# Kernel tuning notes

Hardware: AMD Instinct MI355X
Metric: run time of the kernel (lower is better)

Reference implementation:

```python
import jax, jax.numpy as jnp
import numpy as np

DIM = 256; HEADS = 8; HD = DIM // HEADS; WIN = 3; LOCAL = WIN * WIN
SR = 8; SHARED = 4; ROUTED = 2
B = 4; RES = 64; TBL = 4096
EPS = 1.1920929e-07  # torch.finfo(float32).eps


def _l2(x):
    return x / jnp.clip(jnp.linalg.norm(x, axis=-1, keepdims=True), EPS)


def _forward(x, relative_coords_table, q_w, q_b, kv_w, kv_b, temperature,
             query_embedding, rpb_local, learnable_tokens, learnable_bias,
             cpb1_w, cpb1_b, cpb2_w, cpb2_b, sr_w, sr_b, norm_g, norm_b,
             wg_w, wg0_w, wg1_w, proj_w, proj_b, relative_pos_index, H, W):
    B_, N, C = x.shape
    pH, pW = H // SR, W // SR
    PL = pH * pW
    _x = x.reshape(B_ * N, C)

    # ---- MoE head routing: top-k gating over routed heads ----
    gates = jax.nn.softmax(_x @ wg_w.T, axis=1)                 # (BN, n_routed)
    _, idx = jax.lax.top_k(gates, ROUTED)
    mask = jax.nn.one_hot(idx, gates.shape[1], dtype=gates.dtype).sum(axis=1)
    rg = gates * mask
    rg = rg / jnp.clip(jnp.sum(rg, axis=1, keepdims=True), EPS)
    routed_gates = rg.reshape(B_, N, -1) * ROUTED

    # ---- seq-length-scale buffer: log(local valid-window count + pool_len) ----
    r = WIN // 2
    ch = np.minimum(np.arange(H) + r, H - 1) - np.maximum(np.arange(H) - r, 0) + 1
    cw = np.minimum(np.arange(W) + r, W - 1) - np.maximum(np.arange(W) - r, 0) + 1
    sls = jnp.asarray(np.log(np.outer(ch, cw).reshape(-1, 1).astype(np.float32) + PL))

    # ---- queries ----
    q = (x @ q_w.T + q_b).reshape(B_, N, HEADS, HD).transpose(0, 2, 1, 3)
    q_norm = _l2(q)                                             # (B,h,N,d)
    q_scaled = (q_norm + query_embedding) * jax.nn.softplus(temperature) * sls

    # ---- local branch: unfold normalized k and v over 3x3 windows (zero pad) ----
    kv = x @ kv_w.T + kv_b                                      # (B,N,2C)
    k_loc = _l2(kv[..., :C].reshape(B_, N, HEADS, HD)).reshape(B_, N, C)
    kvl = jnp.concatenate([k_loc, kv[..., C:]], -1).transpose(0, 2, 1).reshape(B_, 2 * C, H, W)
    kvp = jnp.pad(kvl, ((0, 0), (0, 0), (r, r), (r, r)))
    patches = jnp.stack([kvp[:, :, i:i + H, j:j + W] for i in range(WIN) for j in range(WIN)], axis=2)
    patches = patches.reshape(B_, 2 * HEADS, HD, LOCAL, N).transpose(0, 1, 4, 2, 3)  # (B,2h,N,d,L)
    k_local, v_local = patches[:, :HEADS], patches[:, HEADS:]

    attn_local = jnp.einsum('bhnd,bhndl->bhnl', q_scaled, k_local) + rpb_local[:, None, :]

    # ---- pooled global branch ----
    x_ = x.transpose(0, 2, 1).reshape(B_, C, H, W)
    x_ = jnp.einsum('oc,bchw->bohw', sr_w, x_) + sr_b[None, :, None, None]  # 1x1 conv
    x_ = jax.nn.gelu(x_, approximate=False)
    x_ = x_.reshape(B_, C, pH, SR, pW, SR).mean((3, 5)).reshape(B_, C, PL).transpose(0, 2, 1)
    mu = x_.mean(-1, keepdims=True)
    var = ((x_ - mu) ** 2).mean(-1, keepdims=True)
    x_ = (x_ - mu) / jnp.sqrt(var + 1e-5) * norm_g + norm_b
    kvp2 = (x_ @ kv_w.T + kv_b).reshape(B_, PL, 2 * HEADS, HD).transpose(0, 2, 1, 3)
    k_pool, v_pool = kvp2[:, :HEADS], kvp2[:, HEADS:]

    cpb = jax.nn.relu(relative_coords_table @ cpb1_w.T + cpb1_b) @ cpb2_w.T + cpb2_b  # (T,h)
    pool_bias = cpb.T[:, relative_pos_index.reshape(-1)].reshape(HEADS, N, PL)
    attn_pool = jnp.einsum('bhnd,bhpd->bhnp', q_scaled, _l2(k_pool)) + pool_bias

    # ---- joint softmax over local + pooled keys ----
    attn = jax.nn.softmax(jnp.concatenate([attn_local, attn_pool], axis=-1), axis=-1)
    a_loc, a_pool = attn[..., :LOCAL], attn[..., LOCAL:]
    a_loc = jnp.einsum('bhnd,hdl->bhnl', q_norm, learnable_tokens) + learnable_bias + a_loc
    x_local = jnp.einsum('bhnl,bhndl->bhnd', a_loc, v_local)
    x_pool = jnp.einsum('bhnp,bhpd->bhnd', a_pool, v_pool)
    out = (x_local + x_pool).transpose(0, 2, 1, 3)              # (B,N,h,d)

    # ---- combine shared + routed head gates ----
    shared_gates = jax.nn.softmax(_x @ wg1_w.T, axis=1).reshape(B_, N, SHARED) * SHARED
    w0 = jax.nn.softmax(_x @ wg0_w.T, axis=1).reshape(B_, N, 2) * 2
    masked = jnp.concatenate([w0[..., 0:1] * shared_gates, w0[..., 1:2] * routed_gates], axis=-1)
    out = (masked[..., None] * out).reshape(B_, N, C)
    return out @ proj_w.T + proj_b


def setup_inputs() -> dict:
    key = jax.random.key(0)
    ks = jax.random.split(key, 20)
    H = W = RES
    N = H * W
    C = DIM
    PL = (H // SR) * (W // SR)

    def nrm(i, shape, s=0.02):
        return jax.random.normal(ks[i], shape, dtype=jnp.float32) * s

    return {
        'x': jax.random.normal(ks[0], (B, N, C), dtype=jnp.float32),
        'relative_coords_table': jax.random.normal(ks[1], (TBL, 2), dtype=jnp.float32),
        'q_w': nrm(3, (C, C)), 'q_b': jnp.zeros((C,), jnp.float32),
        'kv_w': nrm(4, (2 * C, C)), 'kv_b': jnp.zeros((2 * C,), jnp.float32),
        'temperature': jnp.full((HEADS, 1, 1), float(np.log(np.exp(1 / 0.24) - 1)), jnp.float32),
        'query_embedding': nrm(5, (HEADS, 1, HD)),
        'rpb_local': nrm(6, (HEADS, LOCAL), 0.0004),
        'learnable_tokens': nrm(7, (HEADS, HD, LOCAL)),
        'learnable_bias': jnp.zeros((HEADS, 1, LOCAL), jnp.float32),
        'cpb1_w': nrm(8, (512, 2)), 'cpb1_b': jnp.zeros((512,), jnp.float32),
        'cpb2_w': nrm(9, (HEADS, 512)), 'cpb2_b': jnp.zeros((HEADS,), jnp.float32),
        'sr_w': nrm(10, (C, C)), 'sr_b': jnp.zeros((C,), jnp.float32),
        'norm_g': jnp.ones((C,), jnp.float32), 'norm_b': jnp.zeros((C,), jnp.float32),
        'wg_w': nrm(11, (HEADS - SHARED, C)),
        'wg0_w': nrm(12, (2, C)),
        'wg1_w': nrm(13, (SHARED, C)),
        'proj_w': nrm(14, (C, C)), 'proj_b': jnp.zeros((C,), jnp.float32),
        'relative_pos_index': jax.random.randint(ks[2], (N, PL), 0, TBL, dtype=jnp.int32),
        'H': H, 'W': W,
    }


def reference(x, relative_coords_table, q_w, q_b, kv_w, kv_b, temperature,
              query_embedding, rpb_local, learnable_tokens, learnable_bias,
              cpb1_w, cpb1_b, cpb2_w, cpb2_b, sr_w, sr_b, norm_g, norm_b,
              wg_w, wg0_w, wg1_w, proj_w, proj_b, relative_pos_index, H, W):
    return _forward(x, relative_coords_table, q_w, q_b, kv_w, kv_b, temperature,
                    query_embedding, rpb_local, learnable_tokens, learnable_bias,
                    cpb1_w, cpb1_b, cpb2_w, cpb2_b, sr_w, sr_b, norm_g, norm_b,
                    wg_w, wg0_w, wg1_w, proj_w, proj_b, relative_pos_index, H, W)
```

## Files before the change

### kernel.cpp

```cpp
#include <hip/hip_runtime.h>
#include <math.h>

#define EPSF 1.1920929e-07f

typedef __attribute__((ext_vector_type(8))) short short8;
typedef __attribute__((ext_vector_type(4))) float f32x4;

static __device__ __forceinline__ unsigned short f2bf(float f) {
    unsigned int u = __float_as_uint(f);
    return (unsigned short)((u + 0x7FFFu + ((u >> 16) & 1u)) >> 16);
}
static __device__ __forceinline__ float bf2f(unsigned short u) {
    return __uint_as_float((unsigned int)u << 16);
}

__global__ __launch_bounds__(256) void prep_kernel(
    const float* __restrict__ x,
    const float* __restrict__ wg,  const float* __restrict__ wg0,
    const float* __restrict__ wg1,
    const float* __restrict__ q_w, const float* __restrict__ kv_w,
    const float* __restrict__ sr_w, const float* __restrict__ pw,
    const float* __restrict__ tbl,
    const float* __restrict__ c1w, const float* __restrict__ c1b,
    const float* __restrict__ c2w, const float* __restrict__ c2b,
    unsigned short* __restrict__ xbf, float* __restrict__ gate,
    unsigned short* __restrict__ wcat, unsigned short* __restrict__ pwbf,
    float* __restrict__ kv_wT, float* __restrict__ cpb)
{
    __shared__ float shpad[512];
    const int blk = blockIdx.x;
    const int t   = threadIdx.x;
    if (blk < 4096) {
        const int j = t & 63;
        const int row = (blk << 2) + (t >> 6);
        float4 v = *(const float4*)(x + (size_t)row*256 + j*4);
        ushort4 o;
        o.x = f2bf(v.x); o.y = f2bf(v.y); o.z = f2bf(v.z); o.w = f2bf(v.w);
        *(ushort4*)(xbf + (size_t)row*256 + j*4) = o;
        float d[10];
#pragma unroll
        for (int f = 0; f < 10; ++f) {
            const float* wf = (f < 4) ? (wg + f*256) : (f < 6) ? (wg0 + (f-4)*256)
                                                               : (wg1 + (f-6)*256);
            float4 wv = *(const float4*)(wf + j*4);
            float s = v.x*wv.x + v.y*wv.y + v.z*wv.z + v.w*wv.w;
            s += __shfl_xor(s, 32); s += __shfl_xor(s, 16); s += __shfl_xor(s, 8);
            s += __shfl_xor(s, 4);  s += __shfl_xor(s, 2);  s += __shfl_xor(s, 1);
            d[f] = s;
        }
        if (j == 0) {
            float e[4];
            float m = fmaxf(fmaxf(d[0],d[1]), fmaxf(d[2],d[3]));
            float ssum = 0.f;
            for (int i = 0; i < 4; ++i) { e[i] = expf(d[i]-m); ssum += e[i]; }
            for (int i = 0; i < 4; ++i) e[i] /= ssum;
            int i1 = 0;
            for (int i = 1; i < 4; ++i) if (e[i] > e[i1]) i1 = i;
            int i2 = -1;
            for (int i = 0; i < 4; ++i) if (i != i1 && (i2 < 0 || e[i] > e[i2])) i2 = i;
            float rs = fmaxf(e[i1] + e[i2], EPSF);
            float rg[4] = {0.f,0.f,0.f,0.f};
            rg[i1] = e[i1] / rs * 2.f;
            rg[i2] = e[i2] / rs * 2.f;
            float sh[4];
            float m1 = fmaxf(fmaxf(d[6],d[7]), fmaxf(d[8],d[9]));
            float s1 = 0.f;
            for (int i = 0; i < 4; ++i) { sh[i] = expf(d[6+i]-m1); s1 += sh[i]; }
            float mm = fmaxf(d[4], d[5]);
            float e0 = expf(d[4]-mm), e1 = expf(d[5]-mm);
            float w00 = e0/(e0+e1)*2.f, w01 = e1/(e0+e1)*2.f;
            float* gr = gate + ((size_t)row << 3);
            for (int i = 0; i < 4; ++i) gr[i]   = w00 * (sh[i]/s1*4.f);
            for (int i = 0; i < 4; ++i) gr[4+i] = w01 * rg[i];
        }
    } else if (blk < 4416) {
        const int e = ((blk - 4096)*256 + t)*4;
        if (e < 262144) {
            int n = e >> 8, k = e & 255;
            const float* src = (n < 256) ? (q_w + n*256) :
                               (n < 768) ? (kv_w + (n-256)*256) : (sr_w + (n-768)*256);
            float4 v = *(const float4*)(src + k);
            ushort4 o;
            o.x = f2bf(v.x); o.y = f2bf(v.y); o.z = f2bf(v.z); o.w = f2bf(v.w);
            *(ushort4*)(wcat + e) = o;
        } else {
            int e2 = e - 262144;
            float4 v = *(const float4*)(pw + e2);
            ushort4 o;
            o.x = f2bf(v.x); o.y = f2bf(v.y); o.z = f2bf(v.z); o.w = f2bf(v.w);
            *(ushort4*)(pwbf + e2) = o;
        }
    } else if (blk < 4544) {
        const int e = ((blk - 4416)*256 + t)*4;
        int o = e >> 8, k = e & 255;
        float4 v = *(const float4*)(kv_w + e);
        kv_wT[(k+0)*512 + o] = v.x;
        kv_wT[(k+1)*512 + o] = v.y;
        kv_wT[(k+2)*512 + o] = v.z;
        kv_wT[(k+3)*512 + o] = v.w;
    } else {
        const int r = blk - 4544;
        const float c0 = tbl[(size_t)r*2], c1 = tbl[(size_t)r*2+1];
        for (int i = t; i < 512; i += 256)
            shpad[i] = fmaxf(c0*c1w[i*2] + c1*c1w[i*2+1] + c1b[i], 0.f);
        __syncthreads();
        const int hh = t >> 5, dd = t & 31;
        float s = 0.f;
        for (int i = dd; i < 512; i += 32) s += shpad[i] * c2w[hh*512+i];
        for (int off = 16; off; off >>= 1) s += __shfl_xor(s, off, 32);
        if (dd == 0) cpb[(size_t)hh*4096 + r] = (s + c2b[hh]) * 1.44269504089f;
    }
}

__global__ __launch_bounds__(256) void gemm_mfma(
    const unsigned short* __restrict__ A,
    const unsigned short* __restrict__ W,
    const float* __restrict__ B0, const float* __restrict__ B1,
    const float* __restrict__ B2,
    int r1, int r2, int mode,
    float* __restrict__ C, int ldc,
    unsigned short* __restrict__ qkv,
    const float* __restrict__ temp, const float* __restrict__ qe)
{
    __shared__ __attribute__((aligned(16))) unsigned short Bt[64*264];
    const int m0b = blockIdx.y << 7;
    const int n0  = blockIdx.x << 6;
    const int t   = threadIdx.x;
    const int w   = t >> 6;
    const int col16 = t & 15;
    const int quad  = (t & 63) >> 4;

    const float* Bp; int noff;
    if (n0 < r1)      { Bp = B0; noff = 0;  }
    else if (n0 < r2) { Bp = B1; noff = r1; }
    else              { Bp = B2; noff = r2; }

    short8 afrA[8];
    {
        const unsigned short* ap = A + (size_t)(m0b + w*16 + col16)*256 + quad*8;
#pragma unroll
        for (int kk = 0; kk < 8; ++kk)
            afrA[kk] = *(const short8*)(ap + kk*32);
    }
#pragma unroll
    for (int j = 0; j < 8; ++j) {
        int ci = j*256 + t;
        int r = ci >> 5, c = ci & 31;
        uint4 bv = *(const uint4*)(W + (size_t)(n0 + r)*256 + c*8);
        *(uint4*)(Bt + r*264 + c*8) = bv;
    }
    __syncthreads();

    float bias_c[4];
#pragma unroll
    for (int ct = 0; ct < 4; ++ct)
        bias_c[ct] = Bp[n0 + ct*16 + col16 - noff];

    const int region = n0 >> 8;
    float qe_c[4], spt_c[4];
    if (mode == 0 && region == 0) {
#pragma unroll
        for (int c = 0; c < 4; ++c) {
            int col = n0 + c*16 + col16;
            spt_c[c] = log1pf(expf(temp[(col >> 5) & 7])) * 1.44269504089f;
            qe_c[c]  = qe[col];
        }
    }

    auto epilogue = [&](f32x4* acc, int m0) {
        if (mode == 0) {
#pragma unroll
            for (int reg = 0; reg < 4; ++reg) {
                const int row = m0 + w*16 + quad*4 + reg;
                float v[4];
#pragma unroll
                for (int c = 0; c < 4; ++c) v[c] = acc[c][reg] + bias_c[c];
                if (region <= 1) {
#pragma unroll
                    for (int hp = 0; hp < 2; ++hp) {
                        float s = v[2*hp]*v[2*hp] + v[2*hp+1]*v[2*hp+1];
                        s += __shfl_xor(s, 1); s += __shfl_xor(s, 2);
                        s += __shfl_xor(s, 4); s += __shfl_xor(s, 8);
                        float inv = 1.0f / fmaxf(sqrtf(s), EPSF);
                        v[2*hp]   *= inv;
                        v[2*hp+1] *= inv;
                    }
                }
                if (region == 0) {
                    int n = row & 4095;
                    int y = n >> 6, x = n & 63;
                    int cs = ((y==0||y==63)?2:3) + ((x==0||x==63)?2:3);
                    float sls = (cs == 4) ? 4.2195077052f :
                                (cs == 5) ? 4.2484952420f :
                                            4.2904594411f;
#pragma unroll
                    for (int c = 0; c < 4; ++c)
                        v[c] = (v[c] + qe_c[c]) * (spt_c[c] * sls);
                }
                if (region == 3) {
#pragma unroll
                    for (int c = 0; c < 4; ++c) {
                        float g = 0.5f * v[c] * (1.0f + erff(v[c] * 0.70710678118654752f));
                        C[(size_t)row * ldc + n0 + c*16 + col16] = g;
                    }
                } else {
#pragma unroll
                    for (int c = 0; c < 4; ++c)
                        qkv[(size_t)row * 2048 + n0 + c*16 + col16] = f2bf(v[c]);
                }
            }
        } else {
#pragma unroll
            for (int reg = 0; reg < 4; ++reg) {
                const int row = m0 + w*16 + quad*4 + reg;
#pragma unroll
                for (int c = 0; c < 4; ++c)
                    C[(size_t)row * ldc + n0 + c*16 + col16] = acc[c][reg] + bias_c[c];
            }
        }
    };

    f32x4 acc[4];
#pragma unroll
    for (int ct = 0; ct < 4; ++ct) acc[ct] = (f32x4){0.f, 0.f, 0.f, 0.f};
#pragma unroll
    for (int kk = 0; kk < 8; ++kk) {
#pragma unroll
        for (int ct = 0; ct < 4; ++ct) {
            short8 bf = *(const short8*)(Bt + (ct*16 + col16)*264 + kk*32 + quad*8);
            acc[ct] = __builtin_amdgcn_mfma_f32_16x16x32_bf16(afrA[kk], bf, acc[ct], 0, 0, 0);
        }
    }
    short8 afrB[8];
    {
        const unsigned short* ap = A + (size_t)(m0b + 64 + w*16 + col16)*256 + quad*8;
#pragma unroll
        for (int kk = 0; kk < 8; ++kk)
            afrB[kk] = *(const short8*)(ap + kk*32);
    }
    epilogue(acc, m0b);

#pragma unroll
    for (int ct = 0; ct < 4; ++ct) acc[ct] = (f32x4){0.f, 0.f, 0.f, 0.f};
#pragma unroll
    for (int kk = 0; kk < 8; ++kk) {
#pragma unroll
        for (int ct = 0; ct < 4; ++ct) {
            short8 bf = *(const short8*)(Bt + (ct*16 + col16)*264 + kk*32 + quad*8);
            acc[ct] = __builtin_amdgcn_mfma_f32_16x16x32_bf16(afrB[kk], bf, acc[ct], 0, 0, 0);
        }
    }
    epilogue(acc, m0b + 64);
}

__global__ __launch_bounds__(256) void poolkv_kernel(
    const float* __restrict__ buf,
    const float* __restrict__ g, const float* __restrict__ bb,
    const float* __restrict__ kv_wT, const float* __restrict__ kv_b,
    unsigned short* __restrict__ kpb, unsigned short* __restrict__ vpb)
{
    __shared__ float xs[256];
    __shared__ float red[8];
    const int blk  = blockIdx.x;
    const int half = blk & 1;
    const int bp   = blk >> 1;
    const int b = bp >> 6, p = bp & 63;
    const int py = p >> 3, px = p & 7;
    const int t = threadIdx.x;
    const int lane = t & 63, w = t >> 6;

    float acc = 0.f;
#pragma unroll
    for (int dy = 0; dy < 8; ++dy)
#pragma unroll
        for (int dx = 0; dx < 8; ++dx) {
            int s = ((py*8+dy) << 6) + px*8 + dx;
            acc += buf[(((size_t)(b*4096+s)) << 10) + 768 + t];
        }
    acc *= (1.0f/64.0f);

    float a1 = acc, a2 = acc*acc;
    a1 += __shfl_xor(a1, 32); a2 += __shfl_xor(a2, 32);
    a1 += __shfl_xor(a1, 16); a2 += __shfl_xor(a2, 16);
    a1 += __shfl_xor(a1, 8);  a2 += __shfl_xor(a2, 8);
    a1 += __shfl_xor(a1, 4);  a2 += __shfl_xor(a2, 4);
    a1 += __shfl_xor(a1, 2);  a2 += __shfl_xor(a2, 2);
    a1 += __shfl_xor(a1, 1);  a2 += __shfl_xor(a2, 1);
    if (lane == 0) { red[w] = a1; red[4 + w] = a2; }
    __syncthreads();
    float mu = (red[0]+red[1]+red[2]+red[3]) * (1.0f/256.0f);
    float ms = (red[4]+red[5]+red[6]+red[7]) * (1.0f/256.0f);
    float rstd = rsqrtf(ms - mu*mu + 1e-5f);
    xs[t] = (acc - mu) * rstd * g[t] + bb[t];
    __syncthreads();

    float s = kv_b[half*256 + t];
    const float* wbase = kv_wT + half*256 + t;
#pragma unroll 8
    for (int k = 0; k < 256; ++k)
        s += xs[k] * wbase[(size_t)k*512];

    const int h = t >> 5, dd = t & 31;
    const size_t ob = (size_t)(b*8+h) << 11;
    if (half == 0) {
        float s2 = s*s;
        s2 += __shfl_xor(s2, 1); s2 += __shfl_xor(s2, 2);
        s2 += __shfl_xor(s2, 4); s2 += __shfl_xor(s2, 8);
        s2 += __shfl_xor(s2, 16);
        float invn = 1.0f / fmaxf(sqrtf(s2), EPSF);
        kpb[ob + ((size_t)p << 5) + dd] = f2bf(s * invn);
    } else {
        vpb[ob + ((size_t)dd << 6) + p] = f2bf(s);
    }
}

__global__ __launch_bounds__(256, 5) void attn_mfma(
    const unsigned short* __restrict__ qkv,
    unsigned short* __restrict__ ao,
    const unsigned short* __restrict__ kpb,
    const unsigned short* __restrict__ vpb,
    const float* __restrict__ cpb,
    const int*   __restrict__ rpi,
    const float* __restrict__ temp,
    const float* __restrict__ qe,
    const float* __restrict__ rpb,
    const float* __restrict__ lt,
    const float* __restrict__ lb,
    const float* __restrict__ gate)
{
    __shared__ __attribute__((aligned(16))) unsigned char SMEM[32624];
    unsigned short* U0  = (unsigned short*)SMEM;
    unsigned short* U1  = (unsigned short*)(SMEM + 8960);
    unsigned short* P   = (unsigned short*)(SMEM + 14080);
    unsigned short* LTT = (unsigned short*)(SMEM + 31488);
    float* dqvL = (float*)(SMEM + 32512);
    float* rpbL = (float*)(SMEM + 32576);
    float* cpbL = (float*)P;

    const int tile = blockIdx.x;
    const int h    = blockIdx.y;
    const int b    = blockIdx.z;
    const int ty0  = (tile >> 3) << 3;
    const int tx0  = (tile & 7) << 3;
    const int t    = threadIdx.x;
    const int lane  = t & 63;
    const int w     = t >> 6;
    const int col16 = lane & 15;
    const int quad  = lane >> 4;
    const int s_w   = (20*w) & ~15;

    const int nq = w*16 + col16;
    const int qy = ty0 + (nq >> 3), qx = tx0 + (nq & 7);
    short8 aq = *(const short8*)(qkv +
        ((size_t)(b*4096 + ((qy<<6)|qx)))*2048 + h*32 + quad*8);

    int rpv[4][4];
#pragma unroll
    for (int ct = 0; ct < 4; ++ct) {
        int p = ct*16 + col16;
#pragma unroll
        for (int reg = 0; reg < 4; ++reg) {
            int n = w*16 + quad*4 + reg;
            int y = ty0 + (n >> 3), x = tx0 + (n & 7);
            rpv[ct][reg] = rpi[(size_t)((y << 6) | x)*64 + p];
        }
    }

    for (int i = t; i < 896; i += 256) {
        int r = i >> 3, sg = i & 7;
        uint2 val = {0u, 0u};
        if (r < 100) {
            int y = ty0 + r/10 - 1, x = tx0 + r%10 - 1;
            if (y >= 0 && y < 64 && x >= 0 && x < 64)
                val = *(const uint2*)(qkv +
                    (size_t)(b*4096 + ((y<<6)|x))*2048 + h*32 + 256 + sg*4);
        }
        *(uint2*)(U0 + r*40 + sg*4) = val;
    }
    {
        const unsigned short* src = kpb + (size_t)(b*8+h)*2048;
        for (int i = t; i < 512; i += 256)
            *(uint2*)(U1 + (i >> 3)*40 + (i & 7)*4) = *(const uint2*)(src + i*4);
    }
    const float spt  = log1pf(expf(temp[h]));
    const float sptL = spt * 1.44269504089f;
    if (t >= 64 && t < 80) {
        int j = t - 64;
        float s = 0.f;
        if (j < 9) {
            s = lb[h*9 + j];
            for (int dd = 0; dd < 32; ++dd)
                s -= qe[h*32+dd] * lt[(h*32+dd)*9 + j];
        }
        dqvL[j] = s;
    } else if (t >= 80 && t < 89) {
        rpbL[t-80] = rpb[h*9 + (t-80)] * 1.44269504089f;
    }
    for (int i = t; i < 512; i += 256) {
        int j = i >> 5, dd = i & 31;
        LTT[j*32 + dd] = (j < 9) ? f2bf(lt[(h*32+dd)*9 + j]) : (unsigned short)0;
    }
    {
        const float4* src = (const float4*)(cpb + (size_t)h*4096);
        float4* dst = (float4*)cpbL;
        for (int i = t; i < 1024; i += 256) dst[i] = src[i];
    }
    __syncthreads();

    float pbias[4][4];
#pragma unroll
    for (int ct = 0; ct < 4; ++ct)
#pragma unroll
        for (int reg = 0; reg < 4; ++reg)
            pbias[ct][reg] = cpbL[rpv[ct][reg]];

    f32x4 cl[4], cp[4];
    {
        const f32x4 z = {0.f, 0.f, 0.f, 0.f};
#pragma unroll
        for (int ct = 0; ct < 4; ++ct) {
            short8 bk = *(const short8*)(U0 + (s_w + ct*16 + col16)*40 + quad*8);
            cl[ct] = __builtin_amdgcn_mfma_f32_16x16x32_bf16(aq, bk, z, 0, 0, 0);
        }
#pragma unroll
        for (int ct = 0; ct < 4; ++ct) {
            short8 bp = *(const short8*)(U1 + (ct*16 + col16)*40 + quad*8);
            cp[ct] = __builtin_amdgcn_mfma_f32_16x16x32_bf16(aq, bp, z, 0, 0, 0);
        }
    }
#pragma unroll
    for (int ct = 0; ct < 4; ++ct) {
        int hk = s_w + ct*16 + col16;
        int ky = hk / 10, kx = hk - ky*10;
#pragma unroll
        for (int reg = 0; reg < 4; ++reg) {
            int n = w*16 + quad*4 + reg;
            int dy = ky - (n >> 3), dx = kx - (n & 7);
            bool valid = (dy >= 0 && dy <= 2 && dx >= 0 && dx <= 2);
            cl[ct][reg] = valid ? (cl[ct][reg] + rpbL[dy*3 + dx]) : -1e30f;
        }
    }
#pragma unroll
    for (int ct = 0; ct < 4; ++ct)
#pragma unroll
        for (int reg = 0; reg < 4; ++reg)
            cp[ct][reg] += pbias[ct][reg];

    __syncthreads();

    float inv[4];
#pragma unroll
    for (int reg = 0; reg < 4; ++reg) {
        float m = -1e30f;
#pragma unroll
        for (int ct = 0; ct < 4; ++ct) m = fmaxf(m, cl[ct][reg]);
#pragma unroll
        for (int ct = 0; ct < 4; ++ct) m = fmaxf(m, cp[ct][reg]);
        m = fmaxf(m, __shfl_xor(m, 1)); m = fmaxf(m, __shfl_xor(m, 2));
        m = fmaxf(m, __shfl_xor(m, 4)); m = fmaxf(m, __shfl_xor(m, 8));
        float s = 0.f;
#pragma unroll
        for (int ct = 0; ct < 4; ++ct) {
            float e = exp2f(cl[ct][reg] - m); cl[ct][reg] = e; s += e;
        }
#pragma unroll
        for (int ct = 0; ct < 4; ++ct) {
            float e = exp2f(cp[ct][reg] - m); cp[ct][reg] = e; s += e;
        }
        s += __shfl_xor(s, 1); s += __shfl_xor(s, 2);
        s += __shfl_xor(s, 4); s += __shfl_xor(s, 8);
        inv[reg] = 1.0f / s;
    }
#pragma unroll
    for (int ct = 0; ct < 4; ++ct)
#pragma unroll
        for (int reg = 0; reg < 4; ++reg) {
            int n = w*16 + quad*4 + reg;
            P[n*136 + ct*16 + col16] = f2bf(cl[ct][reg] * inv[reg]);
        }
#pragma unroll
    for (int ct = 0; ct < 4; ++ct)
#pragma unroll
        for (int reg = 0; reg < 4; ++reg) {
            int n = w*16 + quad*4 + reg;
            P[n*136 + 64 + ct*16 + col16] = f2bf(cp[ct][reg] * inv[reg]);
        }
    {
        const f32x4 z = {0.f, 0.f, 0.f, 0.f};
        short8 blt = *(const short8*)(LTT + col16*32 + quad*8);
        f32x4 cd = __builtin_amdgcn_mfma_f32_16x16x32_bf16(aq, blt, z, 0, 0, 0);
        if (col16 < 9) {
            const float iA = 1.0f / (sptL * 4.2195077052f);
            const float iB = 1.0f / (sptL * 4.2484952420f);
            const float iC = 1.0f / (sptL * 4.2904594411f);
            int dy = col16 / 3, dx = col16 - dy*3;
#pragma unroll
            for (int reg = 0; reg < 4; ++reg) {
                int n = w*16 + quad*4 + reg;
                int y = ty0 + (n >> 3), x = tx0 + (n & 7);
                int cs = ((y==0||y==63)?2:3) + ((x==0||x==63)?2:3);
                float isc = (cs == 4) ? iA : (cs == 5) ? iB : iC;
                float ltv = cd[reg] * isc + dqvL[col16];
                int hk = ((n >> 3) + dy)*10 + (n & 7) + dx;
                int pc = hk - s_w;
                P[n*136 + pc] = f2bf(bf2f(P[n*136 + pc]) + ltv);
            }
        }
    }
    __syncthreads();

    float gv[4];
#pragma unroll
    for (int reg = 0; reg < 4; ++reg) {
        int n = w*16 + quad*4 + reg;
        int y = ty0 + (n >> 3), x = tx0 + (n & 7);
        gv[reg] = gate[(((size_t)(b*4096 + ((y<<6)|x))) << 3) + h];
    }
    unsigned short* VT  = U0;
    unsigned short* VPT = U1;
    for (int i = t; i < 896; i += 256) {
        int r = i >> 3, sg = i & 7;
        uint2 val = {0u, 0u};
        if (r < 100) {
            int y = ty0 + r/10 - 1, x = tx0 + r%10 - 1;
            if (y >= 0 && y < 64 && x >= 0 && x < 64)
                val = *(const uint2*)(qkv +
                    (size_t)(b*4096 + ((y<<6)|x))*2048 + h*32 + 512 + sg*4);
        }
        int d0 = sg << 2;
        VT[(d0+0)*136 + r] = (unsigned short)(val.x & 0xffffu);
        VT[(d0+1)*136 + r] = (unsigned short)(val.x >> 16);
        VT[(d0+2)*136 + r] = (unsigned short)(val.y & 0xffffu);
        VT[(d0+3)*136 + r] = (unsigned short)(val.y >> 16);
    }
    {
        const unsigned short* vsrc = vpb + (size_t)(b*8+h)*2048;
        for (int i = t; i < 512; i += 256) {
            int d = i >> 4, p4 = (i & 15) << 2;
            *(uint2*)(VPT + d*72 + p4) = *(const uint2*)(vsrc + d*64 + p4);
        }
    }
    __syncthreads();

    f32x4 o0 = {0.f,0.f,0.f,0.f}, o1 = {0.f,0.f,0.f,0.f};
#pragma unroll
    for (int ks = 0; ks < 4; ++ks) {
        short8 a = *(const short8*)(P + (w*16 + col16)*136 + ks*32 + quad*8);
        short8 b0, b1;
        if (ks < 2) {
            b0 = *(const short8*)(VT + col16*136      + s_w + ks*32 + quad*8);
            b1 = *(const short8*)(VT + (16+col16)*136 + s_w + ks*32 + quad*8);
        } else {
            b0 = *(const short8*)(VPT + col16*72      + (ks-2)*32 + quad*8);
            b1 = *(const short8*)(VPT + (16+col16)*72 + (ks-2)*32 + quad*8);
        }
        o0 = __builtin_amdgcn_mfma_f32_16x16x32_bf16(a, b0, o0, 0, 0, 0);
        o1 = __builtin_amdgcn_mfma_f32_16x16x32_bf16(a, b1, o1, 0, 0, 0);
    }
#pragma unroll
    for (int reg = 0; reg < 4; ++reg) {
        int n = w*16 + quad*4 + reg;
        int y = ty0 + (n >> 3), x = tx0 + (n & 7);
        size_t rowo = (size_t)(b*4096 + ((y<<6)|x))*256 + h*32;
        float g = gv[reg];
        ao[rowo + col16]      = f2bf(o0[reg] * g);
        ao[rowo + 16 + col16] = f2bf(o1[reg] * g);
    }
}

extern "C" void kernel_launch(void* const* d_in, const int* in_sizes, int n_in,
                              void* d_out, int out_size, void* d_ws, size_t ws_size,
                              hipStream_t stream)
{
    const float* x    = (const float*)d_in[0];
    const float* tbl  = (const float*)d_in[1];
    const float* q_w  = (const float*)d_in[2];
    const float* q_b  = (const float*)d_in[3];
    const float* kv_w = (const float*)d_in[4];
    const float* kv_b = (const float*)d_in[5];
    const float* temp = (const float*)d_in[6];
    const float* qe   = (const float*)d_in[7];
    const float* rpb  = (const float*)d_in[8];
    const float* lt   = (const float*)d_in[9];
    const float* lb   = (const float*)d_in[10];
    const float* c1w  = (const float*)d_in[11];
    const float* c1b  = (const float*)d_in[12];
    const float* c2w  = (const float*)d_in[13];
    const float* c2b  = (const float*)d_in[14];
    const float* sr_w = (const float*)d_in[15];
    const float* sr_b = (const float*)d_in[16];
    const float* ng   = (const float*)d_in[17];
    const float* nbias= (const float*)d_in[18];
    const float* wg   = (const float*)d_in[19];
    const float* wg0  = (const float*)d_in[20];
    const float* wg1  = (const float*)d_in[21];
    const float* pw   = (const float*)d_in[22];
    const float* pb   = (const float*)d_in[23];
    const int*   rpi  = (const int*)d_in[24];
    (void)in_sizes; (void)n_in; (void)out_size; (void)ws_size;

    float* buf   = (float*)d_ws;
    unsigned short* qkvb = (unsigned short*)d_ws;
    float* xp    = buf + (size_t)16384*1024;
    float* kpoolf= xp + 65536;
    unsigned short* kpb = (unsigned short*)kpoolf;
    unsigned short* vpb = kpb + 131072;
    float* cpbb  = kpoolf + 131072;
    float* gateb = cpbb + 32768;
    float* kvwT  = gateb + 131072;
    unsigned short* xbf  = (unsigned short*)(kvwT + 131072);
    unsigned short* ao   = xbf;
    unsigned short* wcat = xbf + (size_t)16384*256;
    unsigned short* pwbf = wcat + 262144;
    float* out   = (float*)d_out;

    prep_kernel<<<8640,256,0,stream>>>(x, wg, wg0, wg1, q_w, kv_w, sr_w, pw,
                                       tbl, c1w, c1b, c2w, c2b,
                                       xbf, gateb, wcat, pwbf, kvwT, cpbb);
    gemm_mfma<<<dim3(16,128),256,0,stream>>>(xbf, wcat, q_b, kv_b, sr_b,
                                             256, 768, 0, buf, 1024,
                                             qkvb, temp, qe);
    poolkv_kernel<<<512,256,0,stream>>>(buf, ng, nbias, kvwT, kv_b, kpb, vpb);
    attn_mfma<<<dim3(64,8,4),256,0,stream>>>(qkvb, ao, kpb, vpb, cpbb, rpi,
                                             temp, qe, rpb, lt, lb, gateb);
    gemm_mfma<<<dim3(4,128),256,0,stream>>>(ao, pwbf, pb, pb, pb,
                                            1<<30, 1<<30, 1, out, 256,
                                            (unsigned short*)nullptr, nullptr, nullptr);
}
```

Measured before the change: 222.3 us.

## Vectorize GEMM epilogue stores via column permutation; gather cpb bias directly from global

The GEMM now maps MFMA output columns so each lane owns four contiguous columns (B rows read as 4*col16+ct). Bias, query-embedding loads and the bf16/fp32 output stores can then use 4-wide vector accesses, and the L2-norm reduction needs one fewer shuffle stage. In the attention kernel, the relative-position bias is gathered straight from global memory instead of being staged in LDS, and the gate loads are hoisted early. This removes a 16KB LDS copy and one barrier, in exchange for scattered global gathers.

Measured after the change: 220.7 us. No clear change (-0.7%).

```diff
diff --git a/kernel.cpp b/kernel.cpp
--- a/kernel.cpp
+++ b/kernel.cpp
@@ -129,6 +129,7 @@
     const int w   = t >> 6;
     const int col16 = t & 15;
     const int quad  = (t & 63) >> 4;
+    const int cbase = n0 + 4*col16;
 
     const float* Bp; int noff;
     if (n0 < r1)      { Bp = B0; noff = 0;  }
@@ -151,20 +152,15 @@
     }
     __syncthreads();
 
-    float bias_c[4];
-#pragma unroll
-    for (int ct = 0; ct < 4; ++ct)
-        bias_c[ct] = Bp[n0 + ct*16 + col16 - noff];
+    float4 bias4 = *(const float4*)(Bp + cbase - noff);
+    float bias_c[4] = {bias4.x, bias4.y, bias4.z, bias4.w};
 
     const int region = n0 >> 8;
-    float qe_c[4], spt_c[4];
+    float qe_c[4], sptv = 0.f;
     if (mode == 0 && region == 0) {
-#pragma unroll
-        for (int c = 0; c < 4; ++c) {
-            int col = n0 + c*16 + col16;
-            spt_c[c] = log1pf(expf(temp[(col >> 5) & 7])) * 1.44269504089f;
-            qe_c[c]  = qe[col];
-        }
+        float4 q4 = *(const float4*)(qe + cbase);
+        qe_c[0]=q4.x; qe_c[1]=q4.y; qe_c[2]=q4.z; qe_c[3]=q4.w;
+        sptv = log1pf(expf(temp[(cbase >> 5) & 7])) * 1.44269504089f;
     }
 
     auto epilogue = [&](f32x4* acc, int m0) {
@@ -176,15 +172,12 @@
 #pragma unroll
                 for (int c = 0; c < 4; ++c) v[c] = acc[c][reg] + bias_c[c];
                 if (region <= 1) {
-#pragma unroll
-                    for (int hp = 0; hp < 2; ++hp) {
-                        float s = v[2*hp]*v[2*hp] + v[2*hp+1]*v[2*hp+1];
-                        s += __shfl_xor(s, 1); s += __shfl_xor(s, 2);
-                        s += __shfl_xor(s, 4); s += __shfl_xor(s, 8);
-                        float inv = 1.0f / fmaxf(sqrtf(s), EPSF);
-                        v[2*hp]   *= inv;
-                        v[2*hp+1] *= inv;
-                    }
+                    float s = v[0]*v[0] + v[1]*v[1] + v[2]*v[2] + v[3]*v[3];
+                    s += __shfl_xor(s, 1); s += __shfl_xor(s, 2);
+                    s += __shfl_xor(s, 4);
+                    float inv = 1.0f / fmaxf(sqrtf(s), EPSF);
+#pragma unroll
+                    for (int c = 0; c < 4; ++c) v[c] *= inv;
                 }
                 if (region == 0) {
                     int n = row & 4095;
@@ -195,27 +188,29 @@
                                             4.2904594411f;
 #pragma unroll
                     for (int c = 0; c < 4; ++c)
-                        v[c] = (v[c] + qe_c[c]) * (spt_c[c] * sls);
+                        v[c] = (v[c] + qe_c[c]) * (sptv * sls);
                 }
                 if (region == 3) {
-#pragma unroll
-                    for (int c = 0; c < 4; ++c) {
-                        float g = 0.5f * v[c] * (1.0f + erff(v[c] * 0.70710678118654752f));
-                        C[(size_t)row * ldc + n0 + c*16 + col16] = g;
-                    }
+                    float4 g4;
+                    g4.x = 0.5f*v[0]*(1.0f + erff(v[0]*0.70710678118654752f));
+                    g4.y = 0.5f*v[1]*(1.0f + erff(v[1]*0.70710678118654752f));
+                    g4.z = 0.5f*v[2]*(1.0f + erff(v[2]*0.70710678118654752f));
+                    g4.w = 0.5f*v[3]*(1.0f + erff(v[3]*0.70710678118654752f));
+                    *(float4*)(C + (size_t)row * ldc + cbase) = g4;
                 } else {
-#pragma unroll
-                    for (int c = 0; c < 4; ++c)
-                        qkv[(size_t)row * 2048 + n0 + c*16 + col16] = f2bf(v[c]);
+                    ushort4 o;
+                    o.x = f2bf(v[0]); o.y = f2bf(v[1]);
+                    o.z = f2bf(v[2]); o.w = f2bf(v[3]);
+                    *(ushort4*)(qkv + (size_t)row * 2048 + cbase) = o;
                 }
             }
         } else {
 #pragma unroll
             for (int reg = 0; reg < 4; ++reg) {
                 const int row = m0 + w*16 + quad*4 + reg;
-#pragma unroll
-                for (int c = 0; c < 4; ++c)
-                    C[(size_t)row * ldc + n0 + c*16 + col16] = acc[c][reg] + bias_c[c];
+                float4 o4 = {acc[0][reg] + bias_c[0], acc[1][reg] + bias_c[1],
+                             acc[2][reg] + bias_c[2], acc[3][reg] + bias_c[3]};
+                *(float4*)(C + (size_t)row * ldc + cbase) = o4;
             }
         }
     };
@@ -227,7 +222,7 @@
     for (int kk = 0; kk < 8; ++kk) {
 #pragma unroll
         for (int ct = 0; ct < 4; ++ct) {
-            short8 bf = *(const short8*)(Bt + (ct*16 + col16)*264 + kk*32 + quad*8);
+            short8 bf = *(const short8*)(Bt + (4*col16 + ct)*264 + kk*32 + quad*8);
             acc[ct] = __builtin_amdgcn_mfma_f32_16x16x32_bf16(afrA[kk], bf, acc[ct], 0, 0, 0);
         }
     }
@@ -246,7 +241,7 @@
     for (int kk = 0; kk < 8; ++kk) {
 #pragma unroll
         for (int ct = 0; ct < 4; ++ct) {
-            short8 bf = *(const short8*)(Bt + (ct*16 + col16)*264 + kk*32 + quad*8);
+            short8 bf = *(const short8*)(Bt + (4*col16 + ct)*264 + kk*32 + quad*8);
             acc[ct] = __builtin_amdgcn_mfma_f32_16x16x32_bf16(afrB[kk], bf, acc[ct], 0, 0, 0);
         }
     }
@@ -335,7 +330,6 @@
     unsigned short* LTT = (unsigned short*)(SMEM + 31488);
     float* dqvL = (float*)(SMEM + 32512);
     float* rpbL = (float*)(SMEM + 32576);
-    float* cpbL = (float*)P;
 
     const int tile = blockIdx.x;
     const int h    = blockIdx.y;
@@ -365,6 +359,21 @@
             rpv[ct][reg] = rpi[(size_t)((y << 6) | x)*64 + p];
         }
     }
+    const float* cpbh = cpb + (size_t)h*4096;
+    float pbias[4][4];
+#pragma unroll
+    for (int ct = 0; ct < 4; ++ct)
+#pragma unroll
+        for (int reg = 0; reg < 4; ++reg)
+            pbias[ct][reg] = cpbh[rpv[ct][reg]];
+
+    float gv[4];
+#pragma unroll
+    for (int reg = 0; reg < 4; ++reg) {
+        int n = w*16 + quad*4 + reg;
+        int y = ty0 + (n >> 3), x = tx0 + (n & 7);
+        gv[reg] = gate[(((size_t)(b*4096 + ((y<<6)|x))) << 3) + h];
+    }
 
     for (int i = t; i < 896; i += 256) {
         int r = i >> 3, sg = i & 7;
@@ -400,19 +409,7 @@
         int j = i >> 5, dd = i & 31;
         LTT[j*32 + dd] = (j < 9) ? f2bf(lt[(h*32+dd)*9 + j]) : (unsigned short)0;
     }
-    {
-        const float4* src = (const float4*)(cpb + (size_t)h*4096);
-        float4* dst = (float4*)cpbL;
-        for (int i = t; i < 1024; i += 256) dst[i] = src[i];
-    }
     __syncthreads();
-
-    float pbias[4][4];
-#pragma unroll
-    for (int ct = 0; ct < 4; ++ct)
-#pragma unroll
-        for (int reg = 0; reg < 4; ++reg)
-            pbias[ct][reg] = cpbL[rpv[ct][reg]];
 
     f32x4 cl[4], cp[4];
     {
@@ -445,8 +442,6 @@
 #pragma unroll
         for (int reg = 0; reg < 4; ++reg)
             cp[ct][reg] += pbias[ct][reg];
-
-    __syncthreads();
 
     float inv[4];
 #pragma unroll
@@ -509,13 +504,6 @@
     }
     __syncthreads();
 
-    float gv[4];
-#pragma unroll
-    for (int reg = 0; reg < 4; ++reg) {
-        int n = w*16 + quad*4 + reg;
-        int y = ty0 + (n >> 3), x = tx0 + (n & 7);
-        gv[reg] = gate[(((size_t)(b*4096 + ((y<<6)|x))) << 3) + h];
-    }
     unsigned short* VT  = U0;
     unsigned short* VPT = U1;
     for (int i = t; i < 896; i += 256) {
```
